# Optimization experiments

Measured on AMD Instinct MI355X. Metric: run time of the kernel, lower is better.

The kernel has to match this reference:

```python
import jax, jax.numpy as jnp
import numpy as np

NUM_HEADS = 16
KEY_DIM = 64
B, S, D = 2, 2048, 1024


def setup_inputs() -> dict:
    key = jax.random.key(0)
    ks = jax.random.split(key, 5)
    scale = 1.0 / np.sqrt(D)
    return {
        "x": jax.random.normal(ks[0], (B, S, D), dtype=jnp.float32),
        "Wq": jax.random.normal(ks[1], (D, NUM_HEADS * KEY_DIM), dtype=jnp.float32) * scale,
        "Wk": jax.random.normal(ks[2], (D, NUM_HEADS * KEY_DIM), dtype=jnp.float32) * scale,
        "Wv": jax.random.normal(ks[3], (D, NUM_HEADS * KEY_DIM), dtype=jnp.float32) * scale,
        "Wo": jax.random.normal(ks[4], (NUM_HEADS * KEY_DIM, D), dtype=jnp.float32) * scale,
    }


def reference(x, Wq, Wk, Wv, Wo):
    b, s, d = x.shape
    h, kd = NUM_HEADS, KEY_DIM
    # QKV projections -> [B, H, S, Kd]
    q = (x @ Wq).reshape(b, s, h, kd).transpose(0, 2, 1, 3)
    k = (x @ Wk).reshape(b, s, h, kd).transpose(0, 2, 1, 3)
    v = (x @ Wv).reshape(b, s, h, kd).transpose(0, 2, 1, 3)
    # scaled dot-product attention, full [B,H,S,S] scores (faithful to source)
    logits = jnp.einsum("bhqd,bhkd->bhqk", q, k) / jnp.sqrt(jnp.float32(kd))
    attn = jax.nn.softmax(logits, axis=-1)
    out = jnp.einsum("bhqk,bhkd->bhqd", attn, v)  # [B,H,S,Kd]
    out = out.transpose(0, 2, 1, 3).reshape(b, s, h * kd)
    return out @ Wo
```

## Files before the change

kernel.cpp:

```cpp
#include <hip/hip_runtime.h>


typedef __attribute__((ext_vector_type(8))) short short8;
typedef __attribute__((ext_vector_type(4))) float f32x4;

#define M_ROWS 4096
#define N_COLS 1024
#define K_DIM  1024
#define SEQ    2048

#define QSCALE 0.18033688011111772f

#if defined(__has_builtin)
#if __has_builtin(__builtin_amdgcn_exp2f)
#define EXP2(x) __builtin_amdgcn_exp2f(x)
#endif
#endif
#ifndef EXP2
#define EXP2(x) exp2f(x)
#endif

#define WAITCNT_VM8 0x0F78
#define WAITCNT_VM4 0x0F74

__device__ inline unsigned short f2bf(float f) {
  unsigned int u = __float_as_uint(f);
  u += 0x7fffu + ((u >> 16) & 1u);
  return (unsigned short)(u >> 16);
}

__device__ inline unsigned int cvtpk(float lo, float hi) {
  unsigned int r;
  asm("v_cvt_pk_bf16_f32 %0, %1, %2" : "=v"(r) : "v"(lo), "v"(hi));
  return r;
}

__device__ inline void swap32(unsigned int& a, unsigned int& b) {
  asm("v_permlane32_swap_b32 %0, %1" : "+v"(a), "+v"(b));
}
__device__ inline void swap16(unsigned int& a, unsigned int& b) {
  asm("v_permlane16_swap_b32 %0, %1" : "+v"(a), "+v"(b));
}

__device__ inline void async_load16(const unsigned short* gptr, unsigned short* lptr) {
  __builtin_amdgcn_global_load_lds(
      (const __attribute__((address_space(1))) unsigned int*)gptr,
      (__attribute__((address_space(3))) unsigned int*)lptr, 16, 0, 0);
}

__global__ void detect_kernel(const unsigned short* __restrict__ x, int* __restrict__ flag) {
  __shared__ int bad;
  if (threadIdx.x == 0) bad = 0;
  __syncthreads();
  for (int i = threadIdx.x; i < 1024; i += 256) {
    float f = __uint_as_float((unsigned int)x[i] << 16);
    float a = fabsf(f);
    if (!(a < 1e4f)) atomicOr(&bad, 1);
  }
  __syncthreads();
  if (threadIdx.x == 0) *flag = bad ? 0 : 1;
}

__global__ void convert_kernel(const void* __restrict__ src, unsigned short* __restrict__ dst,
                               int n4, const int* __restrict__ flag) {
  const int isbf = *flag;
  const int stride = gridDim.x * blockDim.x;
  for (int i = blockIdx.x * blockDim.x + threadIdx.x; i < n4; i += stride) {
    if (isbf) {
      ((uint2*)dst)[i] = ((const uint2*)src)[i];
    } else {
      float4 v = ((const float4*)src)[i];
      ushort4 o;
      o.x = f2bf(v.x); o.y = f2bf(v.y); o.z = f2bf(v.z); o.w = f2bf(v.w);
      ((ushort4*)dst)[i] = o;
    }
  }
}

__global__ __launch_bounds__(256) void convert_wT4_kernel(
    const void* __restrict__ s0, const void* __restrict__ s1,
    const void* __restrict__ s2, const void* __restrict__ s3,
    unsigned short* __restrict__ d0, unsigned short* __restrict__ d1,
    unsigned short* __restrict__ d2, unsigned short* __restrict__ d3,
    const int* __restrict__ flag) {
  __shared__ unsigned short t[32][33];
  const int z = blockIdx.z;
  const void* src = (z == 0) ? s0 : (z == 1) ? s1 : (z == 2) ? s2 : s3;
  unsigned short* dst = (z == 0) ? d0 : (z == 1) ? d1 : (z == 2) ? d2 : d3;
  const int tid = threadIdx.x;
  const int r0 = blockIdx.y * 32, c0 = blockIdx.x * 32;
  const int kr = tid >> 3, nc = (tid & 7) * 4;
  if (*flag) {
    const unsigned short* W = (const unsigned short*)src;
    uint2 v = *(const uint2*)(W + (size_t)(r0 + kr) * K_DIM + c0 + nc);
    t[kr][nc] = v.x & 0xffff; t[kr][nc + 1] = v.x >> 16;
    t[kr][nc + 2] = v.y & 0xffff; t[kr][nc + 3] = v.y >> 16;
  } else {
    const float* W = (const float*)src;
    float4 v = *(const float4*)(W + (size_t)(r0 + kr) * K_DIM + c0 + nc);
    t[kr][nc] = f2bf(v.x); t[kr][nc + 1] = f2bf(v.y);
    t[kr][nc + 2] = f2bf(v.z); t[kr][nc + 3] = f2bf(v.w);
  }
  __syncthreads();
  const int nr = tid >> 3, kc = (tid & 7) * 4;
  uint2 w;
  w.x = (unsigned int)t[kc][nr] | ((unsigned int)t[kc + 1][nr] << 16);
  w.y = (unsigned int)t[kc + 2][nr] | ((unsigned int)t[kc + 3][nr] << 16);
  *(uint2*)(dst + (size_t)(c0 + nr) * K_DIM + r0 + kc) = w;
}

#define GEMM_DMA(Aptr, Bptr, KTOT, KB, BUF)                                       \
  _Pragma("unroll") for (int r = 0; r < 2; ++r) {                                 \
    int s = r * 256 + wave * 64 + lane;                                           \
    int row = s >> 2, c = s & 3;                                                  \
    int g = c ^ ((row ^ (row >> 2)) & 3);                                         \
    async_load16((Aptr) + (size_t)(m0 + row) * (KTOT) + (KB) + g * 8,             \
                 &As[BUF][(size_t)(r * 256 + wave * 64) * 8]);                    \
    async_load16((Bptr) + (size_t)(n0 + row) * (KTOT) + (KB) + g * 8,             \
                 &Bs[BUF][(size_t)(r * 256 + wave * 64) * 8]);                    \
  }

#define GEMM_MAIN_LOOP(Aptr, Bptr, KTOT)                                          \
  f32x4 acc[4][4];                                                                \
  _Pragma("unroll") for (int i = 0; i < 4; ++i)                                   \
  _Pragma("unroll") for (int j = 0; j < 4; ++j)                                   \
      acc[i][j] = (f32x4){0.f, 0.f, 0.f, 0.f};                                    \
  const int xr = (l15 ^ (l15 >> 2)) & 3;                                          \
  GEMM_DMA(Aptr, Bptr, KTOT, 0, 0)                                                \
  for (int kb = 0; kb < (KTOT); kb += 32) {                                       \
    const int pp = (kb >> 5) & 1;                                                 \
    const int kbn = (kb + 32) & ((KTOT) - 1);                                     \
    GEMM_DMA(Aptr, Bptr, KTOT, kbn, pp ^ 1)                                       \
    __builtin_amdgcn_s_waitcnt(WAITCNT_VM4);                                      \
    __syncthreads();                                                              \
    short8 am[4], bn[4];                                                          \
    _Pragma("unroll") for (int i = 0; i < 4; ++i) {                               \
      int arow = wr * 64 + i * 16 + l15;                                          \
      int brow = wc * 64 + i * 16 + l15;                                          \
      int cc = quad ^ xr;                                                         \
      am[i] = *(const short8*)(&As[pp][arow * 32 + cc * 8]);                      \
      bn[i] = *(const short8*)(&Bs[pp][brow * 32 + cc * 8]);                      \
    }                                                                             \
    _Pragma("unroll") for (int i = 0; i < 4; ++i)                                 \
    _Pragma("unroll") for (int j = 0; j < 4; ++j)                                 \
        acc[i][j] = __builtin_amdgcn_mfma_f32_16x16x32_bf16(am[i], bn[j],         \
                                                            acc[i][j], 0, 0, 0); \
    __syncthreads();                                                              \
  }

__global__ __launch_bounds__(256, 3) void qkv_gemm_kernel(
    const unsigned short* __restrict__ Xb,
    const unsigned short* __restrict__ Wqt,
    const unsigned short* __restrict__ Wkt,
    const unsigned short* __restrict__ Wvt,
    unsigned short* __restrict__ Qb,
    unsigned short* __restrict__ Kb,
    unsigned short* __restrict__ Vt) {
  __shared__ __align__(16) unsigned short As[2][128 * 32];
  __shared__ __align__(16) unsigned short Bs[2][128 * 32];
  const int tid = threadIdx.x;
  const int wave = tid >> 6, lane = tid & 63;
  const int quad = lane >> 4, l15 = lane & 15;
  const int wr = wave >> 1, wc = wave & 1;
  const int gid = blockIdx.x;
  const int ny = gid & 7;
  const int q = gid >> 3;
  const int wsel = q >> 5;
  const int m0 = (q & 31) * 128;
  const int n0 = ny * 128;
  const unsigned short* __restrict__ Bt =
      (wsel == 0) ? Wqt : ((wsel == 1) ? Wkt : Wvt);

  GEMM_MAIN_LOOP(Xb, Bt, K_DIM)

#pragma unroll
  for (int i = 0; i < 4; ++i) {
#pragma unroll
    for (int j = 0; j < 4; ++j) {
      int mbase = m0 + wr * 64 + i * 16 + quad * 4;
      int n = n0 + wc * 64 + j * 16 + l15;
      int h = n >> 6, d = n & 63;
      if (wsel == 2) {
        int b_ = mbase >> 11, s = mbase & 2047;
        uint2 w;
        w.x = cvtpk(acc[i][j][0], acc[i][j][1]);
        w.y = cvtpk(acc[i][j][2], acc[i][j][3]);
        *(uint2*)(Vt + ((size_t)(b_ * 16 + h) * 64 + d) * SEQ + s) = w;
      } else {
#pragma unroll
        for (int r = 0; r < 4; ++r) {
          int m = mbase + r;
          int b_ = m >> 11, s = m & 2047;
          float val = acc[i][j][r];
          if (wsel == 0)
            Qb[((size_t)(b_ * 16 + h) * SEQ + s) * 64 + d] = f2bf(val * QSCALE);
          else
            Kb[((size_t)(b_ * 16 + h) * SEQ + s) * 64 + d] = f2bf(val);
        }
      }
    }
  }
}

__global__ __launch_bounds__(256, 2) void flash_kernel(
    const unsigned short* __restrict__ Qb,
    const unsigned short* __restrict__ Kb,
    const unsigned short* __restrict__ Vt,
    unsigned short* __restrict__ Ob) {
  __shared__ __align__(16) unsigned short Klds[2][128 * 64];
  __shared__ __align__(16) unsigned short Vlds[2][64 * 128];
  const int tid = threadIdx.x;
  const int wave = tid >> 6, lane = tid & 63;
  const int quad = lane >> 4, l15 = lane & 15;
  const int gid = blockIdx.x;
  const int bh = gid & 31;
  const int qidx = gid >> 5;
  const int qbase = qidx * 128 + wave * 32;

  const unsigned short* __restrict__ Qp = Qb + (size_t)bh * SEQ * 64;
  const unsigned short* __restrict__ Kp = Kb + (size_t)bh * SEQ * 64;
  const unsigned short* __restrict__ Vp = Vt + (size_t)bh * 64 * SEQ;

  short8 qf[2][2];
#pragma unroll
  for (int g = 0; g < 2; ++g)
#pragma unroll
    for (int h = 0; h < 2; ++h)
      qf[g][h] = *(const short8*)(Qp + (size_t)(qbase + g * 16 + l15) * 64 + h * 32 + quad * 8);

  f32x4 O[2][4];
#pragma unroll
  for (int g = 0; g < 2; ++g)
#pragma unroll
    for (int t = 0; t < 4; ++t) O[g][t] = (f32x4){0.f, 0.f, 0.f, 0.f};
  float l_i[2] = {0.f, 0.f};

#define FLASH_DMA(KB, BUF)                                                     \
  _Pragma("unroll") for (int r = 0; r < 4; ++r) {                              \
    int s = r * 256 + tid;                                                     \
    int krow = s >> 3, kc = s & 7;                                             \
    int kg = kc ^ (krow & 7);                                                  \
    async_load16(Kp + (size_t)((KB) + krow) * 64 + kg * 8,                     \
                 &Klds[BUF][(size_t)(r * 256 + wave * 64) * 8]);               \
    int vrow = s >> 4, vc = s & 15;                                            \
    int vg = vc ^ (vrow & 15);                                                 \
    async_load16(Vp + (size_t)vrow * SEQ + (KB) + vg * 8,                      \
                 &Vlds[BUF][(size_t)(r * 256 + wave * 64) * 8]);               \
  }

#define QK_READ(t)                                                             \
  int row = (t) * 16 + l15;                                                    \
  int c0 = quad ^ (row & 7), c1 = (quad + 4) ^ (row & 7);                      \
  short8 k0 = *(const short8*)(&Klds[p][row * 64 + c0 * 8]);                   \
  short8 k1 = *(const short8*)(&Klds[p][row * 64 + c1 * 8]);

#define SOFTMAX_G(SRC, PB, G)                                                  \
  {                                                                            \
    float rs = 0.f;                                                            \
    unsigned int wx[8], wy[8];                                                 \
    _Pragma("unroll") for (int t = 0; t < 8; ++t) {                            \
      float p0 = EXP2(SRC[t][0]);                                              \
      float p1 = EXP2(SRC[t][1]);                                              \
      float p2 = EXP2(SRC[t][2]);                                              \
      float p3 = EXP2(SRC[t][3]);                                              \
      rs += (p0 + p1) + (p2 + p3);                                             \
      wx[t] = cvtpk(p0, p1);                                                   \
      wy[t] = cvtpk(p2, p3);                                                   \
    }                                                                          \
    l_i[G] += rs;                                                              \
    _Pragma("unroll") for (int m = 0; m < 4; ++m) {                            \
      unsigned int a = wx[2 * m], c = wx[2 * m + 1];                           \
      unsigned int b = wy[2 * m], d = wy[2 * m + 1];                           \
      swap32(a, c); swap16(a, c);                \
      swap32(b, d); swap16(b, d);                \
      union { short8 s; unsigned int u[4]; } P;                                \
      P.u[0] = a; P.u[1] = b; P.u[2] = c; P.u[3] = d;                          \
      PB[m] = P.s;                                                             \
    }                                                                          \
  }

#define PV_G(PB, G)                                                            \
  _Pragma("unroll") for (int td = 0; td < 4; ++td) {                           \
    int vrow = td * 16 + l15;                                                  \
    _Pragma("unroll") for (int m = 0; m < 4; ++m) {                            \
      short8 vf = *(const short8*)(&Vlds[p][vrow * 128 +                       \
                                           (((m * 4 + quad) ^ l15) * 8)]);     \
      O[G][td] = __builtin_amdgcn_mfma_f32_16x16x32_bf16(vf, PB[m],            \
                                                         O[G][td], 0, 0, 0);   \
    }                                                                          \
  }

  FLASH_DMA(0, 0)

  for (int kb = 0; kb < SEQ; kb += 128) {
    const int p = (kb >> 7) & 1;
    const int kbn = (kb + 128) & (SEQ - 1);
    FLASH_DMA(kbn, p ^ 1)
    __builtin_amdgcn_s_waitcnt(WAITCNT_VM8);
    __syncthreads();

    f32x4 sT0[8], sT1[8];
    __builtin_amdgcn_s_setprio(1);
#pragma unroll
    for (int t = 0; t < 8; ++t) {
      QK_READ(t)
      sT0[t] = __builtin_amdgcn_mfma_f32_16x16x32_bf16(k0, qf[0][0],
               (f32x4){0.f, 0.f, 0.f, 0.f}, 0, 0, 0);
      sT0[t] = __builtin_amdgcn_mfma_f32_16x16x32_bf16(k1, qf[0][1], sT0[t], 0, 0, 0);
    }
    __builtin_amdgcn_s_setprio(0);

#pragma unroll
    for (int t = 0; t < 8; ++t) {
      QK_READ(t)
      sT1[t] = __builtin_amdgcn_mfma_f32_16x16x32_bf16(k0, qf[1][0],
               (f32x4){0.f, 0.f, 0.f, 0.f}, 0, 0, 0);
      sT1[t] = __builtin_amdgcn_mfma_f32_16x16x32_bf16(k1, qf[1][1], sT1[t], 0, 0, 0);
    }
    short8 pb0[4];
    SOFTMAX_G(sT0, pb0, 0)

    PV_G(pb0, 0)
    short8 pb1[4];
    SOFTMAX_G(sT1, pb1, 1)

    PV_G(pb1, 1)

    __syncthreads();
  }

#pragma unroll
  for (int g = 0; g < 2; ++g) {
    l_i[g] += __shfl_xor(l_i[g], 16);
    l_i[g] += __shfl_xor(l_i[g], 32);
  }

  const int b_ = bh >> 4, h = bh & 15;
#pragma unroll
  for (int g = 0; g < 2; ++g) {
    const float inv = 1.f / l_i[g];
    unsigned short* orow = Ob + ((size_t)(b_ * SEQ) + qbase + g * 16 + l15) * N_COLS + h * 64;
#pragma unroll
    for (int t = 0; t < 4; ++t) {
      uint2 w;
      w.x = cvtpk(O[g][t][0] * inv, O[g][t][1] * inv);
      w.y = cvtpk(O[g][t][2] * inv, O[g][t][3] * inv);
      *(uint2*)(orow + t * 16 + quad * 4) = w;
    }
  }
#undef FLASH_DMA
#undef QK_READ
#undef SOFTMAX_G
#undef PV_G
}

__global__ __launch_bounds__(256, 3) void out_gemm_kernel(
    const unsigned short* __restrict__ Ob,
    const unsigned short* __restrict__ Wot,
    void* __restrict__ out,
    const int* __restrict__ flag) {
  __shared__ __align__(16) unsigned short As[2][128 * 32];
  __shared__ __align__(16) unsigned short Bs[2][128 * 32];
  const int tid = threadIdx.x;
  const int wave = tid >> 6, lane = tid & 63;
  const int quad = lane >> 4, l15 = lane & 15;
  const int wr = wave >> 1, wc = wave & 1;
  const int m0 = blockIdx.x * 128;
  const int n0 = blockIdx.y * 128;
  const int isbf = *flag;

  GEMM_MAIN_LOOP(Ob, Wot, N_COLS)

#pragma unroll
  for (int i = 0; i < 4; ++i) {
#pragma unroll
    for (int j = 0; j < 4; ++j) {
      int mbase = m0 + wr * 64 + i * 16 + quad * 4;
      int n = n0 + wc * 64 + j * 16 + l15;
#pragma unroll
      for (int r = 0; r < 4; ++r) {
        float val = acc[i][j][r];
        if (isbf) ((unsigned short*)out)[(size_t)(mbase + r) * K_DIM + n] = f2bf(val);
        else      ((float*)out)[(size_t)(mbase + r) * K_DIM + n] = val;
      }
    }
  }
}

extern "C" void kernel_launch(void* const* d_in, const int* in_sizes, int n_in,
                              void* d_out, int out_size, void* d_ws, size_t ws_size,
                              hipStream_t stream) {
  const void* x  = d_in[0];
  const void* wq = d_in[1];
  const void* wk = d_in[2];
  const void* wv = d_in[3];
  const void* wo = d_in[4];

  char* ws = (char*)d_ws;
  size_t off = 0;
  int* flag = (int*)(ws + off);                 off += 256;
  unsigned short* xb  = (unsigned short*)(ws + off); off += (size_t)M_ROWS * K_DIM * 2;
  unsigned short* wqt = (unsigned short*)(ws + off); off += (size_t)K_DIM * N_COLS * 2;
  unsigned short* wkt = (unsigned short*)(ws + off); off += (size_t)K_DIM * N_COLS * 2;
  unsigned short* wvt = (unsigned short*)(ws + off); off += (size_t)K_DIM * N_COLS * 2;
  unsigned short* wot = (unsigned short*)(ws + off); off += (size_t)N_COLS * K_DIM * 2;
  unsigned short* Qb  = (unsigned short*)(ws + off); off += (size_t)M_ROWS * 1024 * 2;
  unsigned short* Kb  = (unsigned short*)(ws + off); off += (size_t)M_ROWS * 1024 * 2;
  unsigned short* Vtb = (unsigned short*)(ws + off); off += (size_t)M_ROWS * 1024 * 2;
  unsigned short* Ob  = (unsigned short*)(ws + off); off += (size_t)M_ROWS * N_COLS * 2;
  (void)ws_size; (void)in_sizes; (void)n_in; (void)out_size;

  detect_kernel<<<1, 256, 0, stream>>>((const unsigned short*)x, flag);

  convert_kernel<<<2048, 256, 0, stream>>>(x, xb, (M_ROWS * K_DIM) / 4, flag);
  convert_wT4_kernel<<<dim3(32, 32, 4), 256, 0, stream>>>(wq, wk, wv, wo,
                                                          wqt, wkt, wvt, wot, flag);

  qkv_gemm_kernel<<<768, 256, 0, stream>>>(xb, wqt, wkt, wvt, Qb, Kb, Vtb);
  flash_kernel<<<512, 256, 0, stream>>>(Qb, Kb, Vtb, Ob);
  out_gemm_kernel<<<dim3(32, 8), 256, 0, stream>>>(Ob, wot, d_out, flag);
}
```

Measured before the change: 187.0 us.

## Give each wave private K/V LDS buffers and drop block barriers in flash loop

Each of the four waves now streams its own 32-key K/V tiles into a private double-buffered LDS region, so the block-wide __syncthreads in the attention loop are removed and waves proceed independently. The key tile per step shrinks from 128 to 32 and QK, softmax and PV are interleaved per tile, with both query groups sharing each V fragment read. In exchange, every wave loads the full K/V stream itself, so global/L2 traffic for K and V grows fourfold per block, and the per-step MFMA batches are smaller, which may expose more load latency.

```diff
diff --git a/kernel.cpp b/kernel.cpp
--- a/kernel.cpp
+++ b/kernel.cpp
@@ -207,8 +207,8 @@
     const unsigned short* __restrict__ Kb,
     const unsigned short* __restrict__ Vt,
     unsigned short* __restrict__ Ob) {
-  __shared__ __align__(16) unsigned short Klds[2][128 * 64];
-  __shared__ __align__(16) unsigned short Vlds[2][64 * 128];
+  __shared__ __align__(16) unsigned short Klds[4][2][32 * 64];
+  __shared__ __align__(16) unsigned short Vlds[4][2][64 * 32];
   const int tid = threadIdx.x;
   const int wave = tid >> 6, lane = tid & 63;
   const int quad = lane >> 4, l15 = lane & 15;
@@ -221,6 +221,11 @@
   const unsigned short* __restrict__ Kp = Kb + (size_t)bh * SEQ * 64;
   const unsigned short* __restrict__ Vp = Vt + (size_t)bh * 64 * SEQ;
 
+  unsigned short* const Kl0 = &Klds[wave][0][0];
+  unsigned short* const Kl1 = &Klds[wave][1][0];
+  unsigned short* const Vl0 = &Vlds[wave][0][0];
+  unsigned short* const Vl1 = &Vlds[wave][1][0];
+
   short8 qf[2][2];
 #pragma unroll
   for (int g = 0; g < 2; ++g)
@@ -235,30 +240,21 @@
     for (int t = 0; t < 4; ++t) O[g][t] = (f32x4){0.f, 0.f, 0.f, 0.f};
   float l_i[2] = {0.f, 0.f};
 
-#define FLASH_DMA(KB, BUF)                                                     \
+#define WDMA(KB, KL, VL)                                                       \
   _Pragma("unroll") for (int r = 0; r < 4; ++r) {                              \
-    int s = r * 256 + tid;                                                     \
-    int krow = s >> 3, kc = s & 7;                                             \
+    int krow = r * 8 + (lane >> 3), kc = lane & 7;                             \
     int kg = kc ^ (krow & 7);                                                  \
-    async_load16(Kp + (size_t)((KB) + krow) * 64 + kg * 8,                     \
-                 &Klds[BUF][(size_t)(r * 256 + wave * 64) * 8]);               \
-    int vrow = s >> 4, vc = s & 15;                                            \
-    int vg = vc ^ (vrow & 15);                                                 \
-    async_load16(Vp + (size_t)vrow * SEQ + (KB) + vg * 8,                      \
-                 &Vlds[BUF][(size_t)(r * 256 + wave * 64) * 8]);               \
-  }
-
-#define QK_READ(t)                                                             \
-  int row = (t) * 16 + l15;                                                    \
-  int c0 = quad ^ (row & 7), c1 = (quad + 4) ^ (row & 7);                      \
-  short8 k0 = *(const short8*)(&Klds[p][row * 64 + c0 * 8]);                   \
-  short8 k1 = *(const short8*)(&Klds[p][row * 64 + c1 * 8]);
-
-#define SOFTMAX_G(SRC, PB, G)                                                  \
+    async_load16(Kp + (size_t)((KB) + krow) * 64 + kg * 8, (KL) + r * 512);    \
+    int vrow = r * 16 + (lane >> 2), vc = lane & 3;                            \
+    int vg = vc ^ (vrow & 3);                                                  \
+    async_load16(Vp + (size_t)vrow * SEQ + (KB) + vg * 8, (VL) + r * 512);     \
+  }
+
+#define SM32(SRC, PB, G)                                                       \
   {                                                                            \
     float rs = 0.f;                                                            \
-    unsigned int wx[8], wy[8];                                                 \
-    _Pragma("unroll") for (int t = 0; t < 8; ++t) {                            \
+    unsigned int wx[2], wy[2];                                                 \
+    _Pragma("unroll") for (int t = 0; t < 2; ++t) {                            \
       float p0 = EXP2(SRC[t][0]);                                              \
       float p1 = EXP2(SRC[t][1]);                                              \
       float p2 = EXP2(SRC[t][2]);                                              \
@@ -268,65 +264,58 @@
       wy[t] = cvtpk(p2, p3);                                                   \
     }                                                                          \
     l_i[G] += rs;                                                              \
-    _Pragma("unroll") for (int m = 0; m < 4; ++m) {                            \
-      unsigned int a = wx[2 * m], c = wx[2 * m + 1];                           \
-      unsigned int b = wy[2 * m], d = wy[2 * m + 1];                           \
-      swap32(a, c); swap16(a, c);                \
-      swap32(b, d); swap16(b, d);                \
-      union { short8 s; unsigned int u[4]; } P;                                \
-      P.u[0] = a; P.u[1] = b; P.u[2] = c; P.u[3] = d;                          \
-      PB[m] = P.s;                                                             \
+    unsigned int a = wx[0], c = wx[1], b = wy[0], d = wy[1];                   \
+    swap32(a, c); swap16(a, c);                  \
+    swap32(b, d); swap16(b, d);                  \
+    union { short8 s; unsigned int u[4]; } P;                                  \
+    P.u[0] = a; P.u[1] = b; P.u[2] = c; P.u[3] = d;                            \
+    PB = P.s;                                                                  \
+  }
+
+#define FTILE(KL, VL)                                                          \
+  {                                                                            \
+    f32x4 sT0[2], sT1[2];                                                      \
+    __builtin_amdgcn_s_setprio(1);                                             \
+    _Pragma("unroll") for (int t = 0; t < 2; ++t) {                            \
+      int row = t * 16 + l15;                                                  \
+      int c0 = quad ^ (row & 7), c1 = (quad + 4) ^ (row & 7);                  \
+      short8 k0 = *(const short8*)((KL) + row * 64 + c0 * 8);                  \
+      short8 k1 = *(const short8*)((KL) + row * 64 + c1 * 8);                  \
+      sT0[t] = __builtin_amdgcn_mfma_f32_16x16x32_bf16(k0, qf[0][0],           \
+               (f32x4){0.f, 0.f, 0.f, 0.f}, 0, 0, 0);                          \
+      sT0[t] = __builtin_amdgcn_mfma_f32_16x16x32_bf16(k1, qf[0][1],           \
+                                                       sT0[t], 0, 0, 0);       \
+      sT1[t] = __builtin_amdgcn_mfma_f32_16x16x32_bf16(k0, qf[1][0],           \
+               (f32x4){0.f, 0.f, 0.f, 0.f}, 0, 0, 0);                          \
+      sT1[t] = __builtin_amdgcn_mfma_f32_16x16x32_bf16(k1, qf[1][1],           \
+                                                       sT1[t], 0, 0, 0);       \
     }                                                                          \
-  }
-
-#define PV_G(PB, G)                                                            \
-  _Pragma("unroll") for (int td = 0; td < 4; ++td) {                           \
-    int vrow = td * 16 + l15;                                                  \
-    _Pragma("unroll") for (int m = 0; m < 4; ++m) {                            \
-      short8 vf = *(const short8*)(&Vlds[p][vrow * 128 +                       \
-                                           (((m * 4 + quad) ^ l15) * 8)]);     \
-      O[G][td] = __builtin_amdgcn_mfma_f32_16x16x32_bf16(vf, PB[m],            \
-                                                         O[G][td], 0, 0, 0);   \
+    __builtin_amdgcn_s_setprio(0);                                             \
+    short8 pb0, pb1;                                                           \
+    SM32(sT0, pb0, 0)                                                          \
+    SM32(sT1, pb1, 1)                                                          \
+    __builtin_amdgcn_s_setprio(1);                                             \
+    _Pragma("unroll") for (int td = 0; td < 4; ++td) {                         \
+      int row = td * 16 + l15;                                                 \
+      short8 vf = *(const short8*)((VL) + row * 32 +                           \
+                                   ((quad ^ (row & 3)) * 8));                  \
+      O[0][td] = __builtin_amdgcn_mfma_f32_16x16x32_bf16(vf, pb0,              \
+                                                         O[0][td], 0, 0, 0);   \
+      O[1][td] = __builtin_amdgcn_mfma_f32_16x16x32_bf16(vf, pb1,              \
+                                                         O[1][td], 0, 0, 0);   \
     }                                                                          \
-  }
-
-  FLASH_DMA(0, 0)
-
-  for (int kb = 0; kb < SEQ; kb += 128) {
-    const int p = (kb >> 7) & 1;
-    const int kbn = (kb + 128) & (SEQ - 1);
-    FLASH_DMA(kbn, p ^ 1)
+    __builtin_amdgcn_s_setprio(0);                                             \
+  }
+
+  WDMA(0, Kl0, Vl0)
+
+  for (int kb = 0; kb < SEQ; kb += 64) {
+    WDMA(kb + 32, Kl1, Vl1)
     __builtin_amdgcn_s_waitcnt(WAITCNT_VM8);
-    __syncthreads();
-
-    f32x4 sT0[8], sT1[8];
-    __builtin_amdgcn_s_setprio(1);
-#pragma unroll
-    for (int t = 0; t < 8; ++t) {
-      QK_READ(t)
-      sT0[t] = __builtin_amdgcn_mfma_f32_16x16x32_bf16(k0, qf[0][0],
-               (f32x4){0.f, 0.f, 0.f, 0.f}, 0, 0, 0);
-      sT0[t] = __builtin_amdgcn_mfma_f32_16x16x32_bf16(k1, qf[0][1], sT0[t], 0, 0, 0);
-    }
-    __builtin_amdgcn_s_setprio(0);
-
-#pragma unroll
-    for (int t = 0; t < 8; ++t) {
-      QK_READ(t)
-      sT1[t] = __builtin_amdgcn_mfma_f32_16x16x32_bf16(k0, qf[1][0],
-               (f32x4){0.f, 0.f, 0.f, 0.f}, 0, 0, 0);
-      sT1[t] = __builtin_amdgcn_mfma_f32_16x16x32_bf16(k1, qf[1][1], sT1[t], 0, 0, 0);
-    }
-    short8 pb0[4];
-    SOFTMAX_G(sT0, pb0, 0)
-
-    PV_G(pb0, 0)
-    short8 pb1[4];
-    SOFTMAX_G(sT1, pb1, 1)
-
-    PV_G(pb1, 1)
-
-    __syncthreads();
+    FTILE(Kl0, Vl0)
+    WDMA((kb + 64) & (SEQ - 1), Kl0, Vl0)
+    __builtin_amdgcn_s_waitcnt(WAITCNT_VM8);
+    FTILE(Kl1, Vl1)
   }
 
 #pragma unroll
@@ -348,10 +337,9 @@
       *(uint2*)(orow + t * 16 + quad * 4) = w;
     }
   }
-#undef FLASH_DMA
-#undef QK_READ
-#undef SOFTMAX_G
-#undef PV_G
+#undef WDMA
+#undef SM32
+#undef FTILE
 }
 
 __global__ __launch_bounds__(256, 3) void out_gemm_kernel(
```

Result: slower. 191.8 us (+2.6%).
